# Optimization experiments

Measured on AMD Instinct MI355X. Metric: run time of the kernel, lower is better.

Reference implementation:

```python
import jax, jax.numpy as jnp
import numpy as np

A = 22          # players per frame (11 home + 11 away)
F_IN = 16       # in_channels
HEADS = 4       # gnn_head
C = 128         # gnn_hidden_dim
HID = 256       # lstm_hidden_dim
B, T = 32, 256


def gat_layer(x, W, att_src, att_dst, bias, concat):
    """PyG GATConv on a complete graph with self-loops (dense per-frame attention).
    x: [N, A, Fin]; W: [Fin, H*C]; att_src/att_dst: [H, C]; bias: [H*C] or [C].
    edge_attr is ignored (edge_dim=None in the original constructor)."""
    H = att_src.shape[0]
    N, A_, Fin = x.shape
    h = jnp.einsum('naf,fhc->nahc', x, W.reshape(Fin, H, -1))   # [N,A,H,C]
    a_src = jnp.sum(h * att_src, axis=-1)                        # [N,A,H]
    a_dst = jnp.sum(h * att_dst, axis=-1)                        # [N,A,H]
    e = a_dst[:, :, None, :] + a_src[:, None, :, :]              # [N,i,j,H]
    e = jax.nn.leaky_relu(e, 0.2)
    alpha = jax.nn.softmax(e, axis=2)                            # softmax over sources j
    out = jnp.einsum('nijh,njhc->nihc', alpha, h)                # [N,A,H,C]
    out = out.reshape(N, A_, -1) if concat else out.mean(axis=2)
    return out + bias


def lstm_layer(x, mask, Wih, Whh, bih, bhh):
    """Masked LSTM layer == pack_padded_sequence semantics (state frozen past seq_len).
    x: [B,T,in], mask: [B,T] bool. Returns (outputs [B,T,H], h_last [B,H])."""
    Bb, Tt, _ = x.shape
    H = Whh.shape[1]
    xT = jnp.swapaxes(x, 0, 1)                   # [T,B,in]
    mT = jnp.swapaxes(mask, 0, 1)[..., None]     # [T,B,1]
    h0 = jnp.zeros((Bb, H), x.dtype)
    c0 = jnp.zeros((Bb, H), x.dtype)

    def step(carry, inp):
        h, c = carry
        xt, mt = inp
        g = xt @ Wih.T + h @ Whh.T + bih + bhh
        i, f, gg, o = jnp.split(g, 4, axis=-1)   # torch gate order i,f,g,o
        i = jax.nn.sigmoid(i)
        f = jax.nn.sigmoid(f)
        gg = jnp.tanh(gg)
        o = jax.nn.sigmoid(o)
        c_new = f * c + i * gg
        h_new = o * jnp.tanh(c_new)
        h = jnp.where(mt, h_new, h)
        c = jnp.where(mt, c_new, c)
        return (h, c), h

    (h_last, _), hs = jax.lax.scan(step, (h0, c0), (xT, mT))
    return jnp.swapaxes(hs, 0, 1), h_last


def setup_inputs() -> dict:
    key = jax.random.key(0)
    ks = jax.random.split(key, 24)
    rn = lambda k, shape, fan: jax.random.normal(k, shape, jnp.float32) / np.sqrt(fan)
    inp = {
        'features': jax.random.normal(ks[0], (B, T, A, F_IN), jnp.float32),
        'seq_lengths': jax.random.randint(ks[1], (B,), T // 2, T + 1).astype(jnp.int64),
        # GAT layer 1: in=16 -> heads=4, C=128, concat
        'W1': rn(ks[2], (F_IN, HEADS * C), F_IN),
        'att_src1': rn(ks[3], (HEADS, C), C),
        'att_dst1': rn(ks[4], (HEADS, C), C),
        'b1': jnp.zeros((HEADS * C,), jnp.float32),
        # GAT layer 2: in=512 -> heads=1, C=128, avg
        'W2': rn(ks[5], (HEADS * C, C), HEADS * C),
        'att_src2': rn(ks[6], (1, C), C),
        'att_dst2': rn(ks[7], (1, C), C),
        'b2': jnp.zeros((C,), jnp.float32),
        # LSTM layer 0 (input 128 -> 256) and layer 1 (256 -> 256)
        'Wih0': rn(ks[8], (4 * HID, C), C),
        'Whh0': rn(ks[9], (4 * HID, HID), HID),
        'bih0': jnp.zeros((4 * HID,), jnp.float32),
        'bhh0': jnp.zeros((4 * HID,), jnp.float32),
        'Wih1': rn(ks[10], (4 * HID, HID), HID),
        'Whh1': rn(ks[11], (4 * HID, HID), HID),
        'bih1': jnp.zeros((4 * HID,), jnp.float32),
        'bhh1': jnp.zeros((4 * HID,), jnp.float32),
        # classifier
        'clf_w': rn(ks[12], (1, HID), HID),
        'clf_b': jnp.zeros((1,), jnp.float32),
    }
    return inp


def reference(features, seq_lengths, W1, att_src1, att_dst1, b1,
              W2, att_src2, att_dst2, b2,
              Wih0, Whh0, bih0, bhh0, Wih1, Whh1, bih1, bhh1,
              clf_w, clf_b):
    Bb, Tt, A_, Fin = features.shape
    mask = jnp.arange(Tt)[None, :] < seq_lengths[:, None]          # [B,T]
    x = features.reshape(Bb * Tt, A_, Fin)                          # all frames, vectorized
    x = jax.nn.relu(gat_layer(x, W1, att_src1, att_dst1, b1, True))
    x = jax.nn.relu(gat_layer(x, W2, att_src2, att_dst2, b2, False))
    pooled = x.mean(axis=1).reshape(Bb, Tt, -1)                     # global_mean_pool per frame
    pooled = jnp.where(mask[..., None], pooled, 0.0)                # invalid frames -> 0
    h1, _ = lstm_layer(pooled, mask, Wih0, Whh0, bih0, bhh0)
    _, h_last = lstm_layer(h1, mask, Wih1, Whh1, bih1, bhh1)        # h_n[-1]
    logits = (h_last @ clf_w.T + clf_b).squeeze(-1)                 # [B]
    return logits
```

## Files before the change

kernel.cpp:

```cpp
#include <hip/hip_runtime.h>
#include <math.h>

#define A_PL 22
#define F_IN_ 16
#define T_LEN 256
#define NBLK_SEQ 64

__device__ __forceinline__ float sigmoidf_(float x) { return 1.f / (1.f + __expf(-x)); }

__device__ __forceinline__ void gstore(float* p, float v) {
  __hip_atomic_store(p, v, __ATOMIC_RELAXED, __HIP_MEMORY_SCOPE_AGENT);
}
__device__ __forceinline__ float gload(const float* p) {
  return __hip_atomic_load(p, __ATOMIC_RELAXED, __HIP_MEMORY_SCOPE_AGENT);
}

__device__ __forceinline__ void dwait(unsigned* arr, int tlo, int thi) {
  if (threadIdx.x < 64) {
    const int lane = threadIdx.x;
    int t = (lane < 32) ? tlo : thi;
    if (t < 0) t = 0;
    const unsigned tu = (unsigned)t;
    while (__hip_atomic_load(arr + lane * 32, __ATOMIC_ACQUIRE,
                             __HIP_MEMORY_SCOPE_AGENT) < tu) {
      __builtin_amdgcn_s_sleep(1);
    }
  }
  __syncthreads();
  __builtin_amdgcn_fence(__ATOMIC_ACQUIRE, "agent");
}

__device__ __forceinline__ float dpp_xor1(float v) {
  int r = __builtin_amdgcn_mov_dpp(__builtin_bit_cast(int, v), 0xB1, 0xF, 0xF, true);
  return __builtin_bit_cast(float, r);
}
__device__ __forceinline__ float dpp_xor2(float v) {
  int r = __builtin_amdgcn_mov_dpp(__builtin_bit_cast(int, v), 0x4E, 0xF, 0xF, true);
  return __builtin_bit_cast(float, r);
}
__device__ __forceinline__ float dpp_ror4(float v) {
  int r = __builtin_amdgcn_mov_dpp(__builtin_bit_cast(int, v), 0x124, 0xF, 0xF, true);
  return __builtin_bit_cast(float, r);
}
__device__ __forceinline__ float dpp_ror8(float v) {
  int r = __builtin_amdgcn_mov_dpp(__builtin_bit_cast(int, v), 0x128, 0xF, 0xF, true);
  return __builtin_bit_cast(float, r);
}

__device__ __forceinline__ int read_len(const int* __restrict__ lens, int b) {
  return (lens[1] == 0) ? lens[2 * b] : lens[b];
}

__global__ __launch_bounds__(256) void gat_naive(
    const float* __restrict__ feat, const int* __restrict__ lens,
    const float* __restrict__ W1, const float* __restrict__ as1,
    const float* __restrict__ ad1, const float* __restrict__ b1,
    const float* __restrict__ W2, const float* __restrict__ as2,
    const float* __restrict__ ad2, const float* __restrict__ b2,
    float* __restrict__ xT)
{
  const int n = blockIdx.x;
  const int tid = threadIdx.x;
  const int bb = n >> 8;
  const int tt = n & 255;
  if (tt >= read_len(lens, bb)) {
    if (tid < 128) xT[((size_t)tt * 128 + tid) * 32 + bb] = 0.f;
    return;
  }

  __shared__ float xs[352];
  __shared__ float hbuf[2816];
  __shared__ float x2s[11264];
  __shared__ float asrc[22], adst[22], alpha[484];

  for (int i = tid; i < 352; i += 256) xs[i] = feat[(size_t)n * 352 + i];
  __syncthreads();

  const int c_ = tid & 127;
  const int ap_ = tid >> 7;

  for (int hd = 0; hd < 4; hd++) {
    {
      float wreg[16];
      #pragma unroll
      for (int f = 0; f < 16; f++) wreg[f] = W1[f * 512 + hd * 128 + c_];
      #pragma unroll
      for (int q = 0; q < 11; q++) {
        const int a = ap_ + 2 * q;
        float acc = 0.f;
        #pragma unroll
        for (int f4 = 0; f4 < 4; f4++) {
          const float4 x4 = *(const float4*)(xs + a * 16 + f4 * 4);
          acc += x4.x * wreg[f4 * 4] + x4.y * wreg[f4 * 4 + 1]
               + x4.z * wreg[f4 * 4 + 2] + x4.w * wreg[f4 * 4 + 3];
        }
        hbuf[a * 128 + c_] = acc;
      }
    }
    __syncthreads();
    if (tid < 44) {
      int a = tid >> 1;
      const float* av = (tid & 1) ? ad1 : as1;
      float s = 0.f;
      for (int c = 0; c < 128; c++) s += hbuf[a * 128 + c] * av[hd * 128 + c];
      ((tid & 1) ? adst : asrc)[a] = s;
    }
    __syncthreads();
    if (tid < 22) {
      float ev[22], m = -1e30f;
      for (int j = 0; j < 22; j++) {
        float e = adst[tid] + asrc[j];
        e = (e > 0.f) ? e : 0.2f * e;
        ev[j] = e; if (e > m) m = e;
      }
      float s = 0.f;
      for (int j = 0; j < 22; j++) { ev[j] = __expf(ev[j] - m); s += ev[j]; }
      float inv = 1.f / s;
      for (int j = 0; j < 22; j++) alpha[tid * 22 + j] = ev[j] * inv;
    }
    __syncthreads();
    for (int i = tid; i < 2816; i += 256) {
      int a = i >> 7, c = i & 127;
      float acc = 0.f;
      for (int j = 0; j < 22; j++) acc += alpha[a * 22 + j] * hbuf[j * 128 + c];
      x2s[a * 512 + hd * 128 + c] = fmaxf(acc + b1[hd * 128 + c], 0.f);
    }
    __syncthreads();
  }

  {
    float acc[11];
    #pragma unroll
    for (int q = 0; q < 11; q++) acc[q] = 0.f;
    for (int k = 0; k < 512; k += 4) {
      const float w0 = W2[(size_t)(k + 0) * 128 + c_];
      const float w1 = W2[(size_t)(k + 1) * 128 + c_];
      const float w2 = W2[(size_t)(k + 2) * 128 + c_];
      const float w3 = W2[(size_t)(k + 3) * 128 + c_];
      #pragma unroll
      for (int q = 0; q < 11; q++) {
        const float4 x4 = *(const float4*)(x2s + (ap_ + 2 * q) * 512 + k);
        acc[q] += x4.x * w0 + x4.y * w1 + x4.z * w2 + x4.w * w3;
      }
    }
    #pragma unroll
    for (int q = 0; q < 11; q++) hbuf[(ap_ + 2 * q) * 128 + c_] = acc[q];
  }
  __syncthreads();
  if (tid < 44) {
    int a = tid >> 1;
    const float* av = (tid & 1) ? ad2 : as2;
    float s = 0.f;
    for (int c = 0; c < 128; c++) s += hbuf[a * 128 + c] * av[c];
    ((tid & 1) ? adst : asrc)[a] = s;
  }
  __syncthreads();
  if (tid < 22) {
    float ev[22], m = -1e30f;
    for (int j = 0; j < 22; j++) {
      float e = adst[tid] + asrc[j];
      e = (e > 0.f) ? e : 0.2f * e;
      ev[j] = e; if (e > m) m = e;
    }
    float s = 0.f;
    for (int j = 0; j < 22; j++) { ev[j] = __expf(ev[j] - m); s += ev[j]; }
    float inv = 1.f / s;
    for (int j = 0; j < 22; j++) alpha[tid * 22 + j] = ev[j] * inv;
  }
  __syncthreads();
  if (tid < 128) {
    float s = 0.f;
    for (int a = 0; a < 22; a++) {
      float v = b2[tid];
      for (int j = 0; j < 22; j++) v += alpha[a * 22 + j] * hbuf[j * 128 + tid];
      s += fmaxf(v, 0.f);
    }
    xT[((size_t)tt * 128 + tid) * 32 + bb] = s * (1.f / 22.f);
  }
}

template<int KK>
__device__ __forceinline__ void lstm_body(
    const int j0, const float* __restrict__ xT,
    const float* __restrict__ Wih, const float* __restrict__ Whh,
    const float* __restrict__ bih, const float* __restrict__ bhh,
    const int* __restrict__ lens,
    float* __restrict__ h0T, float* __restrict__ h1T,
    unsigned* __restrict__ arr, const int bid,
    float* __restrict__ wlds, float* __restrict__ hs, float* __restrict__ gates)
{
  constexpr int NK = KK / 16;
  constexpr bool IS1 = (KK == 512);
  const int tid = threadIdx.x;
  const int kp = tid & 15;
  const int cg = (tid >> 4) & 7;
  const int bg = tid >> 7;
  const int c0 = cg * 4;
  const int b0 = bg * 8;
  const int sw = (kp & 7) << 2;
  const float* hpA = hs + kp * 32 + (b0 ^ sw);
  const float* hpB = hs + kp * 32 + ((b0 + 4) ^ sw);
  const float* wp  = wlds + kp * 32 + (c0 ^ sw);

  for (int c = 0; c < 32; c++) {
    const int r = ((c >> 3) << 8) + j0 + (c & 7);
    for (int k = tid; k < KK; k += 512) {
      float v;
      if (IS1) v = (k < 256) ? Wih[r * 256 + k] : Whh[r * 256 + (k - 256)];
      else     v = (k < 128) ? Wih[r * 128 + k] : Whh[r * 256 + (k - 128)];
      wlds[k * 32 + (c ^ ((k & 7) << 2))] = v;
    }
  }

  const int nb = tid >> 3, njl = tid & 7;
  float bb0 = 0.f, bb1 = 0.f, bb2 = 0.f, bb3 = 0.f;
  int len_b = T_LEN;
  if (tid < 256) {
    const int j = j0 + njl;
    bb0 = bih[j]       + bhh[j];
    bb1 = bih[256 + j] + bhh[256 + j];
    bb2 = bih[512 + j] + bhh[512 + j];
    bb3 = bih[768 + j] + bhh[768 + j];
    len_b = read_len(lens, nb);
  }
  float creg = 0.f;

  const int PMAX = IS1 ? T_LEN : (T_LEN - 1);
  for (int p = 0; p <= PMAX; p++) {
    if (p > 0) dwait(arr, p, IS1 ? p : p - 2);
    const bool compute = IS1 ? (p >= 1) : true;

    if (compute) {
      if (IS1) {
        const float* s0 = h0T + (size_t)((p - 1) & 3) * 8192;
        const float* s1 = h1T + (size_t)((p + 2) & 3) * 8192;
        #pragma unroll
        for (int i = tid; i < 4096; i += 512) {
          const int k = i >> 3, b4 = (i & 7) << 2;
          const float4 v = (k < 256)
              ? *(const float4*)(s0 + (k << 5) + b4)
              : *(const float4*)(s1 + ((k - 256) << 5) + b4);
          *(float4*)(hs + (k << 5) + (b4 ^ ((k & 7) << 2))) = v;
        }
      } else {
        const float* xp = xT + (size_t)p * 4096;
        const float* s0 = h0T + (size_t)((p + 3) & 3) * 8192;
        #pragma unroll
        for (int i = tid; i < 3072; i += 512) {
          const int k = i >> 3, b4 = (i & 7) << 2;
          const float4 v = (k < 128)
              ? *(const float4*)(xp + (k << 5) + b4)
              : *(const float4*)(s0 + ((k - 128) << 5) + b4);
          *(float4*)(hs + (k << 5) + (b4 ^ ((k & 7) << 2))) = v;
        }
      }
      __syncthreads();

      float a[4][8] = {};
      #pragma unroll
      for (int t = 0; t < NK; t++) {
        const float4 hA = *(const float4*)(hpA + t * 512);
        const float4 hB = *(const float4*)(hpB + t * 512);
        const float4 wv = *(const float4*)(wp + t * 512);
        const float w4[4] = { wv.x, wv.y, wv.z, wv.w };
        #pragma unroll
        for (int ci = 0; ci < 4; ci++) {
          const float w = w4[ci];
          a[ci][0] += w * hA.x; a[ci][1] += w * hA.y;
          a[ci][2] += w * hA.z; a[ci][3] += w * hA.w;
          a[ci][4] += w * hB.x; a[ci][5] += w * hB.y;
          a[ci][6] += w * hB.z; a[ci][7] += w * hB.w;
        }
      }
      #pragma unroll
      for (int ci = 0; ci < 4; ci++) {
        #pragma unroll
        for (int bi = 0; bi < 8; bi++) {
          float v = a[ci][bi];
          v += dpp_xor1(v);
          v += dpp_xor2(v);
          v += dpp_ror4(v);
          v += dpp_ror8(v);
          a[ci][bi] = v;
        }
      }
      float g0 = 0.f, g1 = 0.f;
      #pragma unroll
      for (int ci = 0; ci < 4; ci++) {
        #pragma unroll
        for (int bq = 0; bq < 4; bq++) {
          if ((kp & 3) == ci && (kp >> 2) == bq) { g0 = a[ci][bq]; g1 = a[ci][bq + 4]; }
        }
      }
      gates[(b0 + (kp >> 2)) * 34 + c0 + (kp & 3)] = g0;
      gates[(b0 + 4 + (kp >> 2)) * 34 + c0 + (kp & 3)] = g1;
      __syncthreads();

      if (tid < 256) {
        const float gi = gates[nb * 34 + njl];
        const float gf = gates[nb * 34 + 8 + njl];
        const float gg = gates[nb * 34 + 16 + njl];
        const float go = gates[nb * 34 + 24 + njl];
        const float iv = sigmoidf_(gi + bb0);
        const float fv = sigmoidf_(gf + bb1);
        const float gv = tanhf(gg + bb2);
        const float ov = sigmoidf_(go + bb3);
        const float cnew = fv * creg + iv * gv;
        const float hnew = ov * tanhf(cnew);
        const int t_eff = IS1 ? (p - 1) : p;
        const bool valid = t_eff < len_b;
        const int kold = (IS1 ? 256 : 128) + j0 + njl;
        const float hold = hs[(kold << 5) + (nb ^ ((kold & 7) << 2))];
        const float houtv = valid ? hnew : hold;
        if (valid) creg = cnew;
        float* dst = (IS1 ? h1T + (size_t)((p + 3) & 3) * 8192
                          : h0T + (size_t)(p & 3) * 8192)
                     + (j0 + njl) * 32 + nb;
        gstore(dst, houtv);
      }
    }

    __syncthreads();
    if (tid == 0)
      __hip_atomic_store(arr + bid * 32, (unsigned)(p + 1), __ATOMIC_RELEASE,
                         __HIP_MEMORY_SCOPE_AGENT);
  }
}

__global__ __launch_bounds__(512) void lstm_pipe(
    const float* __restrict__ xT,
    const float* __restrict__ Wih0, const float* __restrict__ Whh0,
    const float* __restrict__ bih0, const float* __restrict__ bhh0,
    const float* __restrict__ Wih1, const float* __restrict__ Whh1,
    const float* __restrict__ bih1, const float* __restrict__ bhh1,
    const int* __restrict__ lens,
    const float* __restrict__ clfw, const float* __restrict__ clfb,
    float* __restrict__ ws, float* __restrict__ out)
{
  __shared__ float wlds[16384];
  __shared__ float hs[16384];
  __shared__ float gates[32 * 34 + 2];

  unsigned* arr = (unsigned*)ws;
  float* h0T = ws + 2048;
  float* h1T = ws + 2048 + 32768;

  const int bid = blockIdx.x;
  if (bid >= 32)
    lstm_body<512>((bid - 32) * 8, xT, Wih1, Whh1, bih1, bhh1, lens,
                   h0T, h1T, arr, bid, wlds, hs, gates);
  else
    lstm_body<384>(bid * 8, xT, Wih0, Whh0, bih0, bhh0, lens,
                   h0T, h1T, arr, bid, wlds, hs, gates);

  if (bid == 0) {
    const int tid = threadIdx.x;
    dwait(arr, 0, T_LEN + 1);
    const float* h1f = h1T + (size_t)3 * 8192;
    if (tid < 256) {
      const int b = tid & 31, jg = tid >> 5;
      float s = 0.f;
      #pragma unroll 8
      for (int jj = 0; jj < 32; jj++) {
        const int j = jg * 32 + jj;
        s += gload(h1f + j * 32 + b) * clfw[j];
      }
      gates[jg * 32 + b] = s;
    }
    __syncthreads();
    if (tid < 32) {
      float s = clfb[0];
      #pragma unroll
      for (int g = 0; g < 8; g++) s += gates[g * 32 + tid];
      out[tid] = s;
    }
  }
}

extern "C" void kernel_launch(void* const* d_in, const int* in_sizes, int n_in,
                              void* d_out, int out_size, void* d_ws, size_t ws_size,
                              hipStream_t stream) {
  (void)in_sizes; (void)n_in; (void)out_size; (void)ws_size;
  const float* feat = (const float*)d_in[0];
  const int*   lens = (const int*)d_in[1];
  const float* W1   = (const float*)d_in[2];
  const float* as1  = (const float*)d_in[3];
  const float* ad1  = (const float*)d_in[4];
  const float* b1   = (const float*)d_in[5];
  const float* W2   = (const float*)d_in[6];
  const float* as2  = (const float*)d_in[7];
  const float* ad2  = (const float*)d_in[8];
  const float* b2   = (const float*)d_in[9];
  const float* Wih0 = (const float*)d_in[10];
  const float* Whh0 = (const float*)d_in[11];
  const float* bih0 = (const float*)d_in[12];
  const float* bhh0 = (const float*)d_in[13];
  const float* Wih1 = (const float*)d_in[14];
  const float* Whh1 = (const float*)d_in[15];
  const float* bih1 = (const float*)d_in[16];
  const float* bhh1 = (const float*)d_in[17];
  const float* clfw = (const float*)d_in[18];
  const float* clfb = (const float*)d_in[19];

  float* ws  = (float*)d_ws;
  float* xT  = ws + 2048 + 65536;
  float* outp = (float*)d_out;

  hipMemsetAsync(d_ws, 0, (2048 + 65536) * sizeof(float), stream);

  gat_naive<<<8192, 256, 0, stream>>>(feat, lens, W1, as1, ad1, b1,
                                      W2, as2, ad2, b2, xT);

  void* args[] = {
    (void*)&xT,
    (void*)&Wih0, (void*)&Whh0, (void*)&bih0, (void*)&bhh0,
    (void*)&Wih1, (void*)&Whh1, (void*)&bih1, (void*)&bhh1,
    (void*)&lens, (void*)&clfw, (void*)&clfb, (void*)&ws, (void*)&outp
  };
  hipLaunchCooperativeKernel((const void*)lstm_pipe, dim3(NBLK_SEQ), dim3(512),
                             args, 0, stream);
}
```

Before: 3.429 ms.

## Split layer-1 LSTM gate matmul to precompute input half ahead of recurrence

Layer-1 LSTM blocks now compute the Wih·h0 half of the gate product for step p+1 as soon as layer-0 output is ready, waiting only on layer-0 flags. They then wait on layer-1 flags separately to add the Whh·h1 half. This takes the input projection off the serial layer-1 critical path and decouples the two layers' waits, at the cost of extra accumulator registers and an extra barrier per step.

```diff
diff --git a/kernel.cpp b/kernel.cpp
--- a/kernel.cpp
+++ b/kernel.cpp
@@ -22,6 +22,18 @@
     if (t < 0) t = 0;
     const unsigned tu = (unsigned)t;
     while (__hip_atomic_load(arr + lane * 32, __ATOMIC_ACQUIRE,
+                             __HIP_MEMORY_SCOPE_AGENT) < tu) {
+      __builtin_amdgcn_s_sleep(1);
+    }
+  }
+  __syncthreads();
+  __builtin_amdgcn_fence(__ATOMIC_ACQUIRE, "agent");
+}
+
+__device__ __forceinline__ void dwait_half(unsigned* arr, int base, int tgt) {
+  if (threadIdx.x < 32) {
+    const unsigned tu = (unsigned)(tgt < 0 ? 0 : tgt);
+    while (__hip_atomic_load(arr + (base + threadIdx.x) * 32, __ATOMIC_ACQUIRE,
                              __HIP_MEMORY_SCOPE_AGENT) < tu) {
       __builtin_amdgcn_s_sleep(1);
     }
@@ -179,8 +191,7 @@
   }
 }
 
-template<int KK>
-__device__ __forceinline__ void lstm_body(
+__device__ __forceinline__ void lstm_body_l0(
     const int j0, const float* __restrict__ xT,
     const float* __restrict__ Wih, const float* __restrict__ Whh,
     const float* __restrict__ bih, const float* __restrict__ bhh,
@@ -189,8 +200,7 @@
     unsigned* __restrict__ arr, const int bid,
     float* __restrict__ wlds, float* __restrict__ hs, float* __restrict__ gates)
 {
-  constexpr int NK = KK / 16;
-  constexpr bool IS1 = (KK == 512);
+  constexpr int NK = 24;
   const int tid = threadIdx.x;
   const int kp = tid & 15;
   const int cg = (tid >> 4) & 7;
@@ -204,10 +214,8 @@
 
   for (int c = 0; c < 32; c++) {
     const int r = ((c >> 3) << 8) + j0 + (c & 7);
-    for (int k = tid; k < KK; k += 512) {
-      float v;
-      if (IS1) v = (k < 256) ? Wih[r * 256 + k] : Whh[r * 256 + (k - 256)];
-      else     v = (k < 128) ? Wih[r * 128 + k] : Whh[r * 256 + (k - 128)];
+    for (int k = tid; k < 384; k += 512) {
+      float v = (k < 128) ? Wih[r * 128 + k] : Whh[r * 256 + (k - 128)];
       wlds[k * 32 + (c ^ ((k & 7) << 2))] = v;
     }
   }
@@ -225,34 +233,19 @@
   }
   float creg = 0.f;
 
-  const int PMAX = IS1 ? T_LEN : (T_LEN - 1);
-  for (int p = 0; p <= PMAX; p++) {
-    if (p > 0) dwait(arr, p, IS1 ? p : p - 2);
-    const bool compute = IS1 ? (p >= 1) : true;
-
-    if (compute) {
-      if (IS1) {
-        const float* s0 = h0T + (size_t)((p - 1) & 3) * 8192;
-        const float* s1 = h1T + (size_t)((p + 2) & 3) * 8192;
-        #pragma unroll
-        for (int i = tid; i < 4096; i += 512) {
-          const int k = i >> 3, b4 = (i & 7) << 2;
-          const float4 v = (k < 256)
-              ? *(const float4*)(s0 + (k << 5) + b4)
-              : *(const float4*)(s1 + ((k - 256) << 5) + b4);
-          *(float4*)(hs + (k << 5) + (b4 ^ ((k & 7) << 2))) = v;
-        }
-      } else {
-        const float* xp = xT + (size_t)p * 4096;
-        const float* s0 = h0T + (size_t)((p + 3) & 3) * 8192;
-        #pragma unroll
-        for (int i = tid; i < 3072; i += 512) {
-          const int k = i >> 3, b4 = (i & 7) << 2;
-          const float4 v = (k < 128)
-              ? *(const float4*)(xp + (k << 5) + b4)
-              : *(const float4*)(s0 + ((k - 128) << 5) + b4);
-          *(float4*)(hs + (k << 5) + (b4 ^ ((k & 7) << 2))) = v;
-        }
+  for (int p = 0; p <= T_LEN - 1; p++) {
+    if (p > 0) dwait(arr, p, p - 2);
+
+    {
+      const float* xp = xT + (size_t)p * 4096;
+      const float* s0 = h0T + (size_t)((p + 3) & 3) * 8192;
+      #pragma unroll
+      for (int i = tid; i < 3072; i += 512) {
+        const int k = i >> 3, b4 = (i & 7) << 2;
+        const float4 v = (k < 128)
+            ? *(const float4*)(xp + (k << 5) + b4)
+            : *(const float4*)(s0 + ((k - 128) << 5) + b4);
+        *(float4*)(hs + (k << 5) + (b4 ^ ((k & 7) << 2))) = v;
       }
       __syncthreads();
 
@@ -307,17 +300,173 @@
         const float ov = sigmoidf_(go + bb3);
         const float cnew = fv * creg + iv * gv;
         const float hnew = ov * tanhf(cnew);
-        const int t_eff = IS1 ? (p - 1) : p;
-        const bool valid = t_eff < len_b;
-        const int kold = (IS1 ? 256 : 128) + j0 + njl;
+        const bool valid = p < len_b;
+        const int kold = 128 + j0 + njl;
         const float hold = hs[(kold << 5) + (nb ^ ((kold & 7) << 2))];
         const float houtv = valid ? hnew : hold;
         if (valid) creg = cnew;
-        float* dst = (IS1 ? h1T + (size_t)((p + 3) & 3) * 8192
-                          : h0T + (size_t)(p & 3) * 8192)
-                     + (j0 + njl) * 32 + nb;
-        gstore(dst, houtv);
-      }
+        gstore(h0T + (size_t)(p & 3) * 8192 + (j0 + njl) * 32 + nb, houtv);
+      }
+    }
+
+    __syncthreads();
+    if (tid == 0)
+      __hip_atomic_store(arr + bid * 32, (unsigned)(p + 1), __ATOMIC_RELEASE,
+                         __HIP_MEMORY_SCOPE_AGENT);
+  }
+}
+
+__device__ __forceinline__ void lstm_body_l1(
+    const int j0,
+    const float* __restrict__ Wih, const float* __restrict__ Whh,
+    const float* __restrict__ bih, const float* __restrict__ bhh,
+    const int* __restrict__ lens,
+    float* __restrict__ h0T, float* __restrict__ h1T,
+    unsigned* __restrict__ arr, const int bid,
+    float* __restrict__ wlds, float* __restrict__ hs, float* __restrict__ gates)
+{
+  const int tid = threadIdx.x;
+  const int kp = tid & 15;
+  const int cg = (tid >> 4) & 7;
+  const int bg = tid >> 7;
+  const int c0 = cg * 4;
+  const int b0 = bg * 8;
+  const int sw = (kp & 7) << 2;
+  const float* hpA = hs + kp * 32 + (b0 ^ sw);
+  const float* hpB = hs + kp * 32 + ((b0 + 4) ^ sw);
+  const float* wp  = wlds + kp * 32 + (c0 ^ sw);
+
+  for (int c = 0; c < 32; c++) {
+    const int r = ((c >> 3) << 8) + j0 + (c & 7);
+    {
+      const int k = tid;
+      float v = (k < 256) ? Wih[r * 256 + k] : Whh[r * 256 + (k - 256)];
+      wlds[k * 32 + (c ^ ((k & 7) << 2))] = v;
+    }
+  }
+
+  const int nb = tid >> 3, njl = tid & 7;
+  float bb0 = 0.f, bb1 = 0.f, bb2 = 0.f, bb3 = 0.f;
+  int len_b = T_LEN;
+  if (tid < 256) {
+    const int j = j0 + njl;
+    bb0 = bih[j]       + bhh[j];
+    bb1 = bih[256 + j] + bhh[256 + j];
+    bb2 = bih[512 + j] + bhh[512 + j];
+    bb3 = bih[768 + j] + bhh[768 + j];
+    len_b = read_len(lens, nb);
+  }
+  float creg = 0.f;
+  float apv[4][8];
+  float an[4][8];
+
+  for (int p = 0; p <= T_LEN; p++) {
+    if (p < T_LEN) {
+      dwait_half(arr, 0, p + 1);
+      const float* s0 = h0T + (size_t)(p & 3) * 8192;
+      #pragma unroll
+      for (int i = tid; i < 2048; i += 512) {
+        const int k = i >> 3, b4 = (i & 7) << 2;
+        const float4 v = *(const float4*)(s0 + (k << 5) + b4);
+        *(float4*)(hs + (k << 5) + (b4 ^ ((k & 7) << 2))) = v;
+      }
+      __syncthreads();
+      #pragma unroll
+      for (int ci = 0; ci < 4; ci++)
+        #pragma unroll
+        for (int bi = 0; bi < 8; bi++) an[ci][bi] = 0.f;
+      #pragma unroll
+      for (int t = 0; t < 16; t++) {
+        const float4 hA = *(const float4*)(hpA + t * 512);
+        const float4 hB = *(const float4*)(hpB + t * 512);
+        const float4 wv = *(const float4*)(wp + t * 512);
+        const float w4[4] = { wv.x, wv.y, wv.z, wv.w };
+        #pragma unroll
+        for (int ci = 0; ci < 4; ci++) {
+          const float w = w4[ci];
+          an[ci][0] += w * hA.x; an[ci][1] += w * hA.y;
+          an[ci][2] += w * hA.z; an[ci][3] += w * hA.w;
+          an[ci][4] += w * hB.x; an[ci][5] += w * hB.y;
+          an[ci][6] += w * hB.z; an[ci][7] += w * hB.w;
+        }
+      }
+    }
+
+    if (p >= 1) {
+      dwait_half(arr, 32, p);
+      const float* s1 = h1T + (size_t)((p + 2) & 3) * 8192;
+      #pragma unroll
+      for (int i = tid; i < 2048; i += 512) {
+        const int k = i >> 3, b4 = (i & 7) << 2;
+        const int kk = 256 + k;
+        const float4 v = *(const float4*)(s1 + (k << 5) + b4);
+        *(float4*)(hs + (kk << 5) + (b4 ^ ((k & 7) << 2))) = v;
+      }
+      __syncthreads();
+      #pragma unroll
+      for (int t = 16; t < 32; t++) {
+        const float4 hA = *(const float4*)(hpA + t * 512);
+        const float4 hB = *(const float4*)(hpB + t * 512);
+        const float4 wv = *(const float4*)(wp + t * 512);
+        const float w4[4] = { wv.x, wv.y, wv.z, wv.w };
+        #pragma unroll
+        for (int ci = 0; ci < 4; ci++) {
+          const float w = w4[ci];
+          apv[ci][0] += w * hA.x; apv[ci][1] += w * hA.y;
+          apv[ci][2] += w * hA.z; apv[ci][3] += w * hA.w;
+          apv[ci][4] += w * hB.x; apv[ci][5] += w * hB.y;
+          apv[ci][6] += w * hB.z; apv[ci][7] += w * hB.w;
+        }
+      }
+      #pragma unroll
+      for (int ci = 0; ci < 4; ci++) {
+        #pragma unroll
+        for (int bi = 0; bi < 8; bi++) {
+          float v = apv[ci][bi];
+          v += dpp_xor1(v);
+          v += dpp_xor2(v);
+          v += dpp_ror4(v);
+          v += dpp_ror8(v);
+          apv[ci][bi] = v;
+        }
+      }
+      float g0 = 0.f, g1 = 0.f;
+      #pragma unroll
+      for (int ci = 0; ci < 4; ci++) {
+        #pragma unroll
+        for (int bq = 0; bq < 4; bq++) {
+          if ((kp & 3) == ci && (kp >> 2) == bq) { g0 = apv[ci][bq]; g1 = apv[ci][bq + 4]; }
+        }
+      }
+      gates[(b0 + (kp >> 2)) * 34 + c0 + (kp & 3)] = g0;
+      gates[(b0 + 4 + (kp >> 2)) * 34 + c0 + (kp & 3)] = g1;
+      __syncthreads();
+
+      if (tid < 256) {
+        const float gi = gates[nb * 34 + njl];
+        const float gf = gates[nb * 34 + 8 + njl];
+        const float gg = gates[nb * 34 + 16 + njl];
+        const float go = gates[nb * 34 + 24 + njl];
+        const float iv = sigmoidf_(gi + bb0);
+        const float fv = sigmoidf_(gf + bb1);
+        const float gv = tanhf(gg + bb2);
+        const float ov = sigmoidf_(go + bb3);
+        const float cnew = fv * creg + iv * gv;
+        const float hnew = ov * tanhf(cnew);
+        const bool valid = (p - 1) < len_b;
+        const int kold = 256 + j0 + njl;
+        const float hold = hs[(kold << 5) + (nb ^ ((kold & 7) << 2))];
+        const float houtv = valid ? hnew : hold;
+        if (valid) creg = cnew;
+        gstore(h1T + (size_t)((p + 3) & 3) * 8192 + (j0 + njl) * 32 + nb, houtv);
+      }
+    }
+
+    if (p < T_LEN) {
+      #pragma unroll
+      for (int ci = 0; ci < 4; ci++)
+        #pragma unroll
+        for (int bi = 0; bi < 8; bi++) apv[ci][bi] = an[ci][bi];
     }
 
     __syncthreads();
@@ -347,11 +496,11 @@
 
   const int bid = blockIdx.x;
   if (bid >= 32)
-    lstm_body<512>((bid - 32) * 8, xT, Wih1, Whh1, bih1, bhh1, lens,
-                   h0T, h1T, arr, bid, wlds, hs, gates);
+    lstm_body_l1((bid - 32) * 8, Wih1, Whh1, bih1, bhh1, lens,
+                 h0T, h1T, arr, bid, wlds, hs, gates);
   else
-    lstm_body<384>(bid * 8, xT, Wih0, Whh0, bih0, bhh0, lens,
-                   h0T, h1T, arr, bid, wlds, hs, gates);
+    lstm_body_l0(bid * 8, xT, Wih0, Whh0, bih0, bhh0, lens,
+                 h0T, h1T, arr, bid, wlds, hs, gates);
 
   if (bid == 0) {
     const int tid = threadIdx.x;
```

New measurement: 3.804 ms. +10.9%, slower.

## Process all four GAT layer-1 heads at once with shared buffer and float4 aggregation

Applied to the files above, without the earlier changes.

Replaces the sequential per-head loop in the first GAT layer with a single pass that projects all 512 columns, computes attention logits and softmax for all four heads in parallel, and aggregates with float4 vectorised reads. The aggregated output is held in registers and written back in place over the projection buffer, so the separate x2s buffer is dropped. This cuts the number of block barriers and keeps more threads busy in the attention stages that previously used only 22–44 threads. The cost is more live registers (11 float4 accumulators), which may lower occupancy.

```diff
diff --git a/kernel.cpp b/kernel.cpp
--- a/kernel.cpp
+++ b/kernel.cpp
@@ -69,9 +69,10 @@
   }
 
   __shared__ float xs[352];
+  __shared__ float hAll[11264];
   __shared__ float hbuf[2816];
-  __shared__ float x2s[11264];
-  __shared__ float asrc[22], adst[22], alpha[484];
+  __shared__ float asrc[88], adst[88];
+  __shared__ float alpha[1936];
 
   for (int i = tid; i < 352; i += 256) xs[i] = feat[(size_t)n * 352 + i];
   __syncthreads();
@@ -79,14 +80,14 @@
   const int c_ = tid & 127;
   const int ap_ = tid >> 7;
 
-  for (int hd = 0; hd < 4; hd++) {
-    {
+  {
+    #pragma unroll
+    for (int cp = 0; cp < 2; cp++) {
+      const int col = tid + cp * 256;
       float wreg[16];
       #pragma unroll
-      for (int f = 0; f < 16; f++) wreg[f] = W1[f * 512 + hd * 128 + c_];
-      #pragma unroll
-      for (int q = 0; q < 11; q++) {
-        const int a = ap_ + 2 * q;
+      for (int f = 0; f < 16; f++) wreg[f] = W1[f * 512 + col];
+      for (int a = 0; a < 22; a++) {
         float acc = 0.f;
         #pragma unroll
         for (int f4 = 0; f4 < 4; f4++) {
@@ -94,39 +95,66 @@
           acc += x4.x * wreg[f4 * 4] + x4.y * wreg[f4 * 4 + 1]
                + x4.z * wreg[f4 * 4 + 2] + x4.w * wreg[f4 * 4 + 3];
         }
-        hbuf[a * 128 + c_] = acc;
-      }
+        hAll[a * 512 + col] = acc;
+      }
+    }
+  }
+  __syncthreads();
+
+  if (tid < 176) {
+    const int hd = tid / 44, r = tid % 44, a = r >> 1;
+    const float* av = (r & 1) ? ad1 : as1;
+    float s = 0.f;
+    for (int c = 0; c < 128; c++)
+      s += hAll[a * 512 + hd * 128 + c] * av[hd * 128 + c];
+    ((r & 1) ? adst : asrc)[hd * 22 + a] = s;
+  }
+  __syncthreads();
+
+  if (tid < 88) {
+    const int hd = tid / 22, a = tid % 22;
+    float ev[22], m = -1e30f;
+    for (int j = 0; j < 22; j++) {
+      float e = adst[hd * 22 + a] + asrc[hd * 22 + j];
+      e = (e > 0.f) ? e : 0.2f * e;
+      ev[j] = e; if (e > m) m = e;
+    }
+    float s = 0.f;
+    for (int j = 0; j < 22; j++) { ev[j] = __expf(ev[j] - m); s += ev[j]; }
+    float inv = 1.f / s;
+    for (int j = 0; j < 22; j++) alpha[hd * 484 + a * 22 + j] = ev[j] * inv;
+  }
+  __syncthreads();
+
+  {
+    float4 acc[11];
+    #pragma unroll
+    for (int q = 0; q < 11; q++) {
+      const int i = tid + q * 256;
+      const int a = i >> 7, rem = i & 127, hd = rem >> 5, c4 = (rem & 31) << 2;
+      float4 v = make_float4(0.f, 0.f, 0.f, 0.f);
+      for (int j = 0; j < 22; j++) {
+        const float al = alpha[hd * 484 + a * 22 + j];
+        const float4 h4 = *(const float4*)(hAll + j * 512 + hd * 128 + c4);
+        v.x += al * h4.x; v.y += al * h4.y;
+        v.z += al * h4.z; v.w += al * h4.w;
+      }
+      const float4 bv = *(const float4*)(b1 + hd * 128 + c4);
+      v.x = fmaxf(v.x + bv.x, 0.f);
+      v.y = fmaxf(v.y + bv.y, 0.f);
+      v.z = fmaxf(v.z + bv.z, 0.f);
+      v.w = fmaxf(v.w + bv.w, 0.f);
+      acc[q] = v;
     }
     __syncthreads();
-    if (tid < 44) {
-      int a = tid >> 1;
-      const float* av = (tid & 1) ? ad1 : as1;
-      float s = 0.f;
-      for (int c = 0; c < 128; c++) s += hbuf[a * 128 + c] * av[hd * 128 + c];
-      ((tid & 1) ? adst : asrc)[a] = s;
-    }
-    __syncthreads();
-    if (tid < 22) {
-      float ev[22], m = -1e30f;
-      for (int j = 0; j < 22; j++) {
-        float e = adst[tid] + asrc[j];
-        e = (e > 0.f) ? e : 0.2f * e;
-        ev[j] = e; if (e > m) m = e;
-      }
-      float s = 0.f;
-      for (int j = 0; j < 22; j++) { ev[j] = __expf(ev[j] - m); s += ev[j]; }
-      float inv = 1.f / s;
-      for (int j = 0; j < 22; j++) alpha[tid * 22 + j] = ev[j] * inv;
-    }
-    __syncthreads();
-    for (int i = tid; i < 2816; i += 256) {
-      int a = i >> 7, c = i & 127;
-      float acc = 0.f;
-      for (int j = 0; j < 22; j++) acc += alpha[a * 22 + j] * hbuf[j * 128 + c];
-      x2s[a * 512 + hd * 128 + c] = fmaxf(acc + b1[hd * 128 + c], 0.f);
-    }
-    __syncthreads();
-  }
+    #pragma unroll
+    for (int q = 0; q < 11; q++) {
+      const int i = tid + q * 256;
+      const int a = i >> 7, rem = i & 127, hd = rem >> 5, c4 = (rem & 31) << 2;
+      *(float4*)(hAll + a * 512 + hd * 128 + c4) = acc[q];
+    }
+  }
+  __syncthreads();
 
   {
     float acc[11];
@@ -139,7 +167,7 @@
       const float w3 = W2[(size_t)(k + 3) * 128 + c_];
       #pragma unroll
       for (int q = 0; q < 11; q++) {
-        const float4 x4 = *(const float4*)(x2s + (ap_ + 2 * q) * 512 + k);
+        const float4 x4 = *(const float4*)(hAll + (ap_ + 2 * q) * 512 + k);
         acc[q] += x4.x * w0 + x4.y * w1 + x4.z * w2 + x4.w * w3;
       }
     }
```

Result: slower. 3.583 ms (+4.5%).
